# Performance work log

Hardware: AMD Instinct MI355X
Metric: run time of the kernel (lower is better)

The kernel has to match this reference:

```python
import jax, jax.numpy as jnp
import numpy as np

D = 1024      # total input features
R = 32        # number of ragged regions
RMAX = 32     # max region size (padding target)
HIDDEN = [128, 128]
H1, H2 = HIDDEN
B = 8192      # batch size


def _made_masks(r, rmax, hidden):
    """TFP AutoregressiveNetwork masks (left-to-right order, 'equal' hidden degrees,
    params=2, use_bias=False), zero-padded to rmax features."""
    order = np.arange(1, r + 1)
    degs = [order]
    for u in hidden:
        mn = min(int(degs[-1].min()), r - 1)
        degs.append(np.maximum(mn, np.ceil(np.arange(1, u + 1) * (r - 1) / float(u + 1)).astype(np.int64)))
    m1 = np.zeros((rmax, hidden[0]), bool)
    m1[:r] = degs[0][:, None] <= degs[1][None, :]
    m2 = degs[1][:, None] <= degs[2][None, :]
    mout = np.zeros((hidden[-1], rmax * 2), bool)
    out_deg = np.repeat(order, 2)  # output layout is feature-major: [feat, param]
    mout[:, :2 * r] = degs[-1][:, None] < out_deg[None, :]
    return m1, m2, mout


def setup_inputs() -> dict:
    rng = np.random.default_rng(0)
    perm = rng.permutation(D)
    sizes = rng.integers(8, RMAX + 1, size=R)
    idx = np.zeros((R, RMAX), np.int64)
    valid = np.zeros((R, RMAX), bool)
    M1 = np.zeros((R, RMAX, H1), bool)
    M2 = np.zeros((R, H1, H2), bool)
    Mout = np.zeros((R, H2, RMAX * 2), bool)
    pos = 0
    for i in range(R):
        s = int(sizes[i])
        idx[i, :s] = perm[pos:pos + s]
        pos += s
        valid[i, :s] = True
        M1[i], M2[i], Mout[i] = _made_masks(s, RMAX, HIDDEN)
    key = jax.random.key(0)
    k1, k2, k3, k4 = jax.random.split(key, 4)
    inputs = jax.random.normal(k1, (B, D), jnp.float32)
    W1 = jax.random.normal(k2, (R, RMAX, H1), jnp.float32) / np.float32(np.sqrt(RMAX))
    W2 = jax.random.normal(k3, (R, H1, H2), jnp.float32) / np.float32(np.sqrt(H1))
    Wout = jax.random.normal(k4, (R, H2, RMAX * 2), jnp.float32) / np.float32(np.sqrt(H2))
    return {"inputs": inputs, "W1": W1, "W2": W2, "Wout": Wout,
            "idx": jnp.asarray(idx), "valid": jnp.asarray(valid),
            "M1": jnp.asarray(M1), "M2": jnp.asarray(M2), "Mout": jnp.asarray(Mout)}


def reference(inputs, W1, W2, Wout, idx, valid, M1, M2, Mout):
    f = inputs.dtype
    v = valid.astype(f)                              # [R, RMAX]
    xg = jnp.take(inputs, idx, axis=1) * v           # [B, R, RMAX] ragged gather (padded)
    # MADE masked MLP (relu, no bias), batched over all regions at once
    h1 = jax.nn.relu(jnp.einsum('brd,rdh->brh', xg, W1 * M1.astype(f)))
    h2 = jax.nn.relu(jnp.einsum('brh,rhk->brk', h1, W2 * M2.astype(f)))
    out = jnp.einsum('brk,rko->bro', h2, Wout * Mout.astype(f))
    out = out.reshape(out.shape[0], out.shape[1], RMAX, 2)
    shift, log_s = out[..., 0], out[..., 1]
    # MAF inverse: u = (x - shift) * exp(-log_scale); logdet = -sum(log_scale)
    u = (xg - shift) * jnp.exp(-log_s)
    elem = -0.5 * u * u - 0.5 * jnp.log(2.0 * jnp.pi) - log_s
    ll = jnp.sum(elem * v, axis=-1)                  # [B, R]
    return ll[..., None]                             # [B, R, 1] as in tf.stack of expand_dims
```

## Files before the change

### kernel.cpp

```cpp
#include <hip/hip_runtime.h>
#include <math.h>


#define RR 32
#define DD 1024
#define HH 128
#define OO 64
#define TROWS 32
#define TILES_PER_BLOCK 16
#define BLOCKS_PER_R 16

#define SHP 136
#define SXG 40
#define SXF 38
#define SSC 132

typedef short bf16x8_t __attribute__((ext_vector_type(8)));
typedef float f32x4_t __attribute__((ext_vector_type(4)));
typedef unsigned short u16;
typedef unsigned int u32;

__device__ __forceinline__ u16 bf16_rne(float x) {
    u32 u = __float_as_uint(x);
    u += 0x7FFFu + ((u >> 16) & 1u);
    return (u16)(u >> 16);
}
__device__ __forceinline__ float bf16_tof(u16 h) {
    return __uint_as_float(((u32)h) << 16);
}
__device__ __forceinline__ u16 lo_trunc(float v, u16 h) {
    return (u16)(__float_as_uint(v - bf16_tof(h)) >> 16);
}
__device__ __forceinline__ u32 pack_split(float v) {
    u16 h = bf16_rne(v);
    return (u32)h | ((u32)lo_trunc(v, h) << 16);
}
__device__ __forceinline__ void unpack8(const u32* p, bf16x8_t& hi, bf16x8_t& lo) {
    uint4 a = *reinterpret_cast<const uint4*>(p);
    uint4 b = *reinterpret_cast<const uint4*>(p + 4);
    union { u32 u[4]; bf16x8_t v; } H, L;
    H.u[0] = __builtin_amdgcn_perm(a.y, a.x, 0x05040100u);
    H.u[1] = __builtin_amdgcn_perm(a.w, a.z, 0x05040100u);
    H.u[2] = __builtin_amdgcn_perm(b.y, b.x, 0x05040100u);
    H.u[3] = __builtin_amdgcn_perm(b.w, b.z, 0x05040100u);
    L.u[0] = __builtin_amdgcn_perm(a.y, a.x, 0x07060302u);
    L.u[1] = __builtin_amdgcn_perm(a.w, a.z, 0x07060302u);
    L.u[2] = __builtin_amdgcn_perm(b.y, b.x, 0x07060302u);
    L.u[3] = __builtin_amdgcn_perm(b.w, b.z, 0x07060302u);
    hi = H.v; lo = L.v;
}
__device__ __forceinline__ f32x4_t mfma16(bf16x8_t a, bf16x8_t b, f32x4_t c) {
    return __builtin_amdgcn_mfma_f32_16x16x32_bf16(a, b, c, 0, 0, 0);
}

__device__ __forceinline__ void stage_block(const float* __restrict__ W,
                                            const int* __restrict__ M,
                                            int ldc, int c0, int K, u32* dst, int sd,
                                            int tid)
{
    const int kb = tid >> 3;
    const int cb = tid & 7;
    if (kb * 4 >= K) return;
    const int k0 = kb * 4;
    float e[4][4];
#pragma unroll
    for (int i = 0; i < 4; ++i) {
        const int o = ((k0 + i) * ldc + c0 + 4 * cb) >> 2;
        float4 w = ((const float4*)W)[o];
        int4   m = ((const int4*)M)[o];
        e[i][0] = m.x ? w.x : 0.f; e[i][1] = m.y ? w.y : 0.f;
        e[i][2] = m.z ? w.z : 0.f; e[i][3] = m.w ? w.w : 0.f;
    }
#pragma unroll
    for (int j = 0; j < 4; ++j) {
        uint4 p;
        p.x = pack_split(e[0][j]); p.y = pack_split(e[1][j]);
        p.z = pack_split(e[2][j]); p.w = pack_split(e[3][j]);
        *(uint4*)&dst[(4 * cb + j) * sd + k0] = p;
    }
}

__device__ __forceinline__ void relu_pack_store(u16* __restrict__ h, u16* __restrict__ l,
                                                int o, f32x4_t a)
{
    float v0 = fmaxf(a[0], 0.f), v1 = fmaxf(a[1], 0.f);
    float v2 = fmaxf(a[2], 0.f), v3 = fmaxf(a[3], 0.f);
    ushort4 vh, vl;
    vh.x = bf16_rne(v0); vl.x = lo_trunc(v0, vh.x);
    vh.y = bf16_rne(v1); vl.y = lo_trunc(v1, vh.y);
    vh.z = bf16_rne(v2); vl.z = lo_trunc(v2, vh.z);
    vh.w = bf16_rne(v3); vl.w = lo_trunc(v3, vh.w);
    *(ushort4*)&h[o] = vh;
    *(ushort4*)&l[o] = vl;
}

__global__ __launch_bounds__(512, 4)
void made_flow_r10(const float* __restrict__ inputs,
                   const float* __restrict__ W1,
                   const float* __restrict__ W2,
                   const float* __restrict__ Wout,
                   const int* __restrict__ idx,
                   const int* __restrict__ valid,
                   const int* __restrict__ M1,
                   const int* __restrict__ M2,
                   const int* __restrict__ Mout,
                   float* __restrict__ out)
{
    __shared__ __align__(16) char regA[TROWS * SHP * 2 * 2];
    __shared__ __align__(16) char regB[TROWS * SHP * 2 * 2];
    __shared__ __align__(16) u16  xgh[2][TROWS * SXG];
    __shared__ __align__(16) u16  xgl[2][TROWS * SXG];
    __shared__ __align__(16) float xgf[2][TROWS * SXF];
    __shared__ __align__(16) float red_all[TILES_PER_BLOCK][TROWS][4];
    __shared__ int   idx_s[RR];
    __shared__ float v_s[RR];

    u16* const h1h = (u16*)regA;
    u16* const h1l = h1h + TROWS * SHP;
    u32* const scr  = (u32*)regA;
    u32* const scr2 = (u32*)regB;
    u16* const h2h = (u16*)regB;
    u16* const h2l = h2h + TROWS * SHP;

    const int tid  = threadIdx.x;
    const int r    = blockIdx.x / BLOCKS_PER_R;
    const int rb   = blockIdx.x % BLOCKS_PER_R;
    const int lane = tid & 63;
    const int wave = tid >> 6;
    const int q    = lane >> 4;
    const int l16  = lane & 15;
    const int wm3  = wave & 3;
    const int ni3  = wave >> 2;

    if (tid < RR) {
        idx_s[tid] = idx[r * RR + tid];
        v_s[tid]   = valid[r * RR + tid] ? 1.f : 0.f;
    }

    bf16x8_t a1h, a1l;
    bf16x8_t a2h[4], a2l[4];
    bf16x8_t aoh[4], aol[4];
    {
        const float* W1r = W1 + r * RR * HH;   const int* M1r = M1 + r * RR * HH;
        const float* W2r = W2 + r * HH * HH;   const int* M2r = M2 + r * HH * HH;
        const float* Wor = Wout + r * HH * OO; const int* Mor = Mout + r * HH * OO;
        const int c = wave >> 1, h = wave & 1;
        for (int i = 0; i < 2; ++i) {
            __syncthreads();
            if (tid < 256) stage_block(W2r, M2r, HH, 32 * (2 * i),     HH, scr,  SSC, tid);
            else           stage_block(W2r, M2r, HH, 32 * (2 * i + 1), HH, scr2, SSC, tid - 256);
            __syncthreads();
            if (c == 2 * i) {
#pragma unroll
                for (int ks = 0; ks < 4; ++ks)
                    unpack8(&scr[(16 * h + l16) * SSC + ks * 32 + q * 8], a2h[ks], a2l[ks]);
            } else if (c == 2 * i + 1) {
#pragma unroll
                for (int ks = 0; ks < 4; ++ks)
                    unpack8(&scr2[(16 * h + l16) * SSC + ks * 32 + q * 8], a2h[ks], a2l[ks]);
            }
        }
        {
            __syncthreads();
            if (tid < 256) stage_block(Wor, Mor, OO, 0,  HH, scr,  SSC, tid);
            else           stage_block(Wor, Mor, OO, 32, HH, scr2, SSC, tid - 256);
            __syncthreads();
            const u32* s = (wm3 >> 1) ? scr2 : scr;
#pragma unroll
            for (int ks = 0; ks < 4; ++ks)
                unpack8(&s[(16 * (wm3 & 1) + l16) * SSC + ks * 32 + q * 8], aoh[ks], aol[ks]);
        }
        for (int i = 0; i < 2; ++i) {
            __syncthreads();
            if (tid < 256) stage_block(W1r, M1r, HH, 32 * (2 * i),     RR, scr,  SSC, tid);
            else           stage_block(W1r, M1r, HH, 32 * (2 * i + 1), RR, scr2, SSC, tid - 256);
            __syncthreads();
            if (c == 2 * i)          unpack8(&scr [(16 * h + l16) * SSC + q * 8], a1h, a1l);
            else if (c == 2 * i + 1) unpack8(&scr2[(16 * h + l16) * SSC + q * 8], a1h, a1l);
        }
    }
    __syncthreads();

    const f32x4_t zero4 = {0.f, 0.f, 0.f, 0.f};
    const int grow = tid >> 4;
    const int gg   = tid & 15;

    {
        const int base = (rb * TILES_PER_BLOCK * TROWS + grow) * DD;
        float gx0 = inputs[base + idx_s[2 * gg]]     * v_s[2 * gg];
        float gx1 = inputs[base + idx_s[2 * gg + 1]] * v_s[2 * gg + 1];
        ushort2 gh, gl;
        gh.x = bf16_rne(gx0); gl.x = lo_trunc(gx0, gh.x);
        gh.y = bf16_rne(gx1); gl.y = lo_trunc(gx1, gh.y);
        *(ushort2*)&xgh[0][grow * SXG + 2 * gg] = gh;
        *(ushort2*)&xgl[0][grow * SXG + 2 * gg] = gl;
        *(float2*)&xgf[0][grow * SXF + 2 * gg] = make_float2(gx0, gx1);
    }
    __syncthreads();

    {
        bf16x8_t bh[2], bl[2];
#pragma unroll
        for (int ni = 0; ni < 2; ++ni) {
            bh[ni] = *(const bf16x8_t*)&xgh[0][(16 * ni + l16) * SXG + q * 8];
            bl[ni] = *(const bf16x8_t*)&xgl[0][(16 * ni + l16) * SXG + q * 8];
        }
#pragma unroll
        for (int ni = 0; ni < 2; ++ni) {
            f32x4_t a = zero4;
            a = mfma16(a1h, bh[ni], a);
            a = mfma16(a1l, bh[ni], a);
            a = mfma16(a1h, bl[ni], a);
            relu_pack_store(h1h, h1l, (16 * ni + l16) * SHP + 16 * wave + 4 * q, a);
        }
    }

    for (int t = 0; t < TILES_PER_BLOCK; ++t) {
        const int row0 = (rb * TILES_PER_BLOCK + t) * TROWS;
        __syncthreads();

        float gx0, gx1;
        const bool dg = (t + 1 < TILES_PER_BLOCK);
        if (dg) {
            const int base = (row0 + TROWS + grow) * DD;
            gx0 = inputs[base + idx_s[2 * gg]]     * v_s[2 * gg];
            gx1 = inputs[base + idx_s[2 * gg + 1]] * v_s[2 * gg + 1];
        }
        {
            f32x4_t acc[2] = {zero4, zero4};
#pragma unroll
            for (int ks = 0; ks < 4; ++ks) {
#pragma unroll
                for (int ni = 0; ni < 2; ++ni) {
                    bf16x8_t bh = *(const bf16x8_t*)&h1h[(16 * ni + l16) * SHP + ks * 32 + q * 8];
                    bf16x8_t bl = *(const bf16x8_t*)&h1l[(16 * ni + l16) * SHP + ks * 32 + q * 8];
                    f32x4_t a = acc[ni];
                    a = mfma16(a2h[ks], bh, a);
                    a = mfma16(a2l[ks], bh, a);
                    a = mfma16(a2h[ks], bl, a);
                    acc[ni] = a;
                }
            }
            if (dg) {
                const int b = (t + 1) & 1;
                ushort2 gh, gl;
                gh.x = bf16_rne(gx0); gl.x = lo_trunc(gx0, gh.x);
                gh.y = bf16_rne(gx1); gl.y = lo_trunc(gx1, gh.y);
                *(ushort2*)&xgh[b][grow * SXG + 2 * gg] = gh;
                *(ushort2*)&xgl[b][grow * SXG + 2 * gg] = gl;
                *(float2*)&xgf[b][grow * SXF + 2 * gg] = make_float2(gx0, gx1);
            }
#pragma unroll
            for (int ni = 0; ni < 2; ++ni)
                relu_pack_store(h2h, h2l, (16 * ni + l16) * SHP + 16 * wave + 4 * q, acc[ni]);
        }
        __syncthreads();

        f32x4_t acc3 = zero4;
#pragma unroll
        for (int ks = 0; ks < 4; ++ks) {
            bf16x8_t bh = *(const bf16x8_t*)&h2h[(16 * ni3 + l16) * SHP + ks * 32 + q * 8];
            bf16x8_t bl = *(const bf16x8_t*)&h2l[(16 * ni3 + l16) * SHP + ks * 32 + q * 8];
            acc3 = mfma16(aoh[ks], bh, acc3);
            acc3 = mfma16(aol[ks], bh, acc3);
            acc3 = mfma16(aoh[ks], bl, acc3);
        }

        if (dg) {
            const int b = (t + 1) & 1;
            bf16x8_t bh[2], bl[2];
#pragma unroll
            for (int ni = 0; ni < 2; ++ni) {
                bh[ni] = *(const bf16x8_t*)&xgh[b][(16 * ni + l16) * SXG + q * 8];
                bl[ni] = *(const bf16x8_t*)&xgl[b][(16 * ni + l16) * SXG + q * 8];
            }
#pragma unroll
            for (int ni = 0; ni < 2; ++ni) {
                f32x4_t a = zero4;
                a = mfma16(a1h, bh[ni], a);
                a = mfma16(a1l, bh[ni], a);
                a = mfma16(a1h, bl[ni], a);
                relu_pack_store(h1h, h1l, (16 * ni + l16) * SHP + 16 * wave + 4 * q, a);
            }
        }

        {
            const int j0 = 8 * wm3 + 2 * q;
            const float vj0 = v_s[j0], vj1 = v_s[j0 + 1];
            const int row = 16 * ni3 + l16;
            float2 xv = *(const float2*)&xgf[t & 1][row * SXF + j0];
            const float u0 = (xv.x - acc3[0]) * __expf(-acc3[1]);
            const float u1 = (xv.y - acc3[2]) * __expf(-acc3[3]);
            float p = (-0.5f * u0 * u0 - 0.91893853320467266954f - acc3[1]) * vj0
                    + (-0.5f * u1 * u1 - 0.91893853320467266954f - acc3[3]) * vj1;
            p += __shfl_xor(p, 16, 64);
            p += __shfl_xor(p, 32, 64);
            if (q == 0) red_all[t][row][wm3] = p;
        }
    }

    __syncthreads();
    {
        const int tt  = tid >> 5;
        const int row = tid & 31;
        float4 rv = *(const float4*)&red_all[tt][row][0];
        out[((rb * TILES_PER_BLOCK + tt) * TROWS + row) * RR + r] =
            rv.x + rv.y + rv.z + rv.w;
    }
}

extern "C" void kernel_launch(void* const* d_in, const int* in_sizes, int n_in,
                              void* d_out, int out_size, void* d_ws, size_t ws_size,
                              hipStream_t stream)
{
    const float* inputs = (const float*)d_in[0];
    const float* W1     = (const float*)d_in[1];
    const float* W2     = (const float*)d_in[2];
    const float* Wout   = (const float*)d_in[3];
    const int*   idx    = (const int*)d_in[4];
    const int*   valid  = (const int*)d_in[5];
    const int*   M1     = (const int*)d_in[6];
    const int*   M2     = (const int*)d_in[7];
    const int*   Mout   = (const int*)d_in[8];
    float*       out    = (float*)d_out;

    hipLaunchKernelGGL(made_flow_r10, dim3(RR * BLOCKS_PER_R), dim3(512), 0, stream,
                       inputs, W1, W2, Wout, idx, valid, M1, M2, Mout, out);
}
```

Baseline: 137.8 us.

## Prefetch gathered inputs two tiles ahead and use hardware bf16 packing

Moves the global gather of the next input tile so it is issued two tiles ahead, right after the second barrier, which gives the loads more time to arrive before they are packed into shared memory. Replaces the software round-to-nearest bf16 conversion with the v_cvt_pk_bf16_f32 instruction plus a perm to extract the low residual, cutting ALU work in the hi/lo split. Also hoists the idx and valid values out of shared memory into registers. This raises register pressure, and the hardware conversion's rounding may differ slightly from the manual RNE for special values.

```diff
diff --git a/kernel.cpp b/kernel.cpp
--- a/kernel.cpp
+++ b/kernel.cpp
@@ -34,6 +34,11 @@
 __device__ __forceinline__ u32 pack_split(float v) {
     u16 h = bf16_rne(v);
     return (u32)h | ((u32)lo_trunc(v, h) << 16);
+}
+__device__ __forceinline__ u32 cvtpk2(float a, float b) {
+    u32 d;
+    asm("v_cvt_pk_bf16_f32 %0, %1, %2" : "=v"(d) : "v"(a), "v"(b));
+    return d;
 }
 __device__ __forceinline__ void unpack8(const u32* p, bf16x8_t& hi, bf16x8_t& lo) {
     uint4 a = *reinterpret_cast<const uint4*>(p);
@@ -85,17 +90,33 @@
 {
     float v0 = fmaxf(a[0], 0.f), v1 = fmaxf(a[1], 0.f);
     float v2 = fmaxf(a[2], 0.f), v3 = fmaxf(a[3], 0.f);
-    ushort4 vh, vl;
-    vh.x = bf16_rne(v0); vl.x = lo_trunc(v0, vh.x);
-    vh.y = bf16_rne(v1); vl.y = lo_trunc(v1, vh.y);
-    vh.z = bf16_rne(v2); vl.z = lo_trunc(v2, vh.z);
-    vh.w = bf16_rne(v3); vl.w = lo_trunc(v3, vh.w);
-    *(ushort4*)&h[o] = vh;
-    *(ushort4*)&l[o] = vl;
+    u32 h01 = cvtpk2(v0, v1);
+    u32 h23 = cvtpk2(v2, v3);
+    float r0 = v0 - __uint_as_float(h01 << 16);
+    float r1 = v1 - __uint_as_float(h01 & 0xffff0000u);
+    float r2 = v2 - __uint_as_float(h23 << 16);
+    float r3 = v3 - __uint_as_float(h23 & 0xffff0000u);
+    u32 l01 = __builtin_amdgcn_perm(__float_as_uint(r1), __float_as_uint(r0), 0x07060302u);
+    u32 l23 = __builtin_amdgcn_perm(__float_as_uint(r3), __float_as_uint(r2), 0x07060302u);
+    uint2 hv; hv.x = h01; hv.y = h23;
+    uint2 lv; lv.x = l01; lv.y = l23;
+    *(uint2*)&h[o] = hv;
+    *(uint2*)&l[o] = lv;
+}
+
+__device__ __forceinline__ void pack2_store(u16* __restrict__ h, u16* __restrict__ l,
+                                            int o, float x0, float x1)
+{
+    u32 h01 = cvtpk2(x0, x1);
+    float r0 = x0 - __uint_as_float(h01 << 16);
+    float r1 = x1 - __uint_as_float(h01 & 0xffff0000u);
+    u32 l01 = __builtin_amdgcn_perm(__float_as_uint(r1), __float_as_uint(r0), 0x07060302u);
+    *(u32*)&h[o] = h01;
+    *(u32*)&l[o] = l01;
 }
 
 __global__ __launch_bounds__(512, 4)
-void made_flow_r10(const float* __restrict__ inputs,
+void made_flow_r11(const float* __restrict__ inputs,
                    const float* __restrict__ W1,
                    const float* __restrict__ W2,
                    const float* __restrict__ Wout,
@@ -185,15 +206,14 @@
     const int grow = tid >> 4;
     const int gg   = tid & 15;
 
-    {
-        const int base = (rb * TILES_PER_BLOCK * TROWS + grow) * DD;
-        float gx0 = inputs[base + idx_s[2 * gg]]     * v_s[2 * gg];
-        float gx1 = inputs[base + idx_s[2 * gg + 1]] * v_s[2 * gg + 1];
-        ushort2 gh, gl;
-        gh.x = bf16_rne(gx0); gl.x = lo_trunc(gx0, gh.x);
-        gh.y = bf16_rne(gx1); gl.y = lo_trunc(gx1, gh.y);
-        *(ushort2*)&xgh[0][grow * SXG + 2 * gg] = gh;
-        *(ushort2*)&xgl[0][grow * SXG + 2 * gg] = gl;
+    const int   ci0 = idx_s[2 * gg], ci1 = idx_s[2 * gg + 1];
+    const float cv0 = v_s[2 * gg],   cv1 = v_s[2 * gg + 1];
+    const int   gbase = (rb * TILES_PER_BLOCK * TROWS + grow) * DD;
+
+    {
+        float gx0 = inputs[gbase + ci0] * cv0;
+        float gx1 = inputs[gbase + ci1] * cv1;
+        pack2_store(xgh[0], xgl[0], grow * SXG + 2 * gg, gx0, gx1);
         *(float2*)&xgf[0][grow * SXF + 2 * gg] = make_float2(gx0, gx1);
     }
     __syncthreads();
@@ -215,17 +235,16 @@
         }
     }
 
+    float gx0, gx1;
+    {
+        gx0 = inputs[gbase + TROWS * DD + ci0] * cv0;
+        gx1 = inputs[gbase + TROWS * DD + ci1] * cv1;
+    }
+
     for (int t = 0; t < TILES_PER_BLOCK; ++t) {
-        const int row0 = (rb * TILES_PER_BLOCK + t) * TROWS;
         __syncthreads();
 
-        float gx0, gx1;
         const bool dg = (t + 1 < TILES_PER_BLOCK);
-        if (dg) {
-            const int base = (row0 + TROWS + grow) * DD;
-            gx0 = inputs[base + idx_s[2 * gg]]     * v_s[2 * gg];
-            gx1 = inputs[base + idx_s[2 * gg + 1]] * v_s[2 * gg + 1];
-        }
         {
             f32x4_t acc[2] = {zero4, zero4};
 #pragma unroll
@@ -243,11 +262,7 @@
             }
             if (dg) {
                 const int b = (t + 1) & 1;
-                ushort2 gh, gl;
-                gh.x = bf16_rne(gx0); gl.x = lo_trunc(gx0, gh.x);
-                gh.y = bf16_rne(gx1); gl.y = lo_trunc(gx1, gh.y);
-                *(ushort2*)&xgh[b][grow * SXG + 2 * gg] = gh;
-                *(ushort2*)&xgl[b][grow * SXG + 2 * gg] = gl;
+                pack2_store(xgh[b], xgl[b], grow * SXG + 2 * gg, gx0, gx1);
                 *(float2*)&xgf[b][grow * SXF + 2 * gg] = make_float2(gx0, gx1);
             }
 #pragma unroll
@@ -255,6 +270,12 @@
                 relu_pack_store(h2h, h2l, (16 * ni + l16) * SHP + 16 * wave + 4 * q, acc[ni]);
         }
         __syncthreads();
+
+        if (t + 2 < TILES_PER_BLOCK) {
+            const int base = gbase + (t + 2) * (TROWS * DD);
+            gx0 = inputs[base + ci0] * cv0;
+            gx1 = inputs[base + ci1] * cv1;
+        }
 
         f32x4_t acc3 = zero4;
 #pragma unroll
@@ -324,6 +345,6 @@
     const int*   Mout   = (const int*)d_in[8];
     float*       out    = (float*)d_out;
 
-    hipLaunchKernelGGL(made_flow_r10, dim3(RR * BLOCKS_PER_R), dim3(512), 0, stream,
+    hipLaunchKernelGGL(made_flow_r11, dim3(RR * BLOCKS_PER_R), dim3(512), 0, stream,
                        inputs, W1, W2, Wout, idx, valid, M1, M2, Mout, out);
 }
```

Result: no change. 135.9 us (-1.3%).
